# Performance work log

Hardware: AMD Instinct MI355X
Metric: run time of the kernel (lower is better)

## Reference

```python
import jax, jax.numpy as jnp
import numpy as np

N = 4096        # num_node == num_hyperedge
IN_FT = 512
OUT_FT = 512
COS_THR = 0.5
COS_K = 10
SCALER = 1.0
EPS = 1e-12  # torch F.normalize eps


def _kaiming_uniform(key, shape, fan_in, a=2.0):
    # kaiming_uniform_ with a=sqrt(4)=2: gain = sqrt(2/(1+a^2)), bound = gain*sqrt(3/fan_in)
    gain = np.sqrt(2.0 / (1.0 + a * a))
    bound = gain * np.sqrt(3.0 / fan_in)
    return jax.random.uniform(key, shape, jnp.float32, -bound, bound)


def setup_inputs() -> dict:
    key = jax.random.key(0)
    k_x, k_w1, k_w2, k_pw, k_pb = jax.random.split(key, 5)
    x = jax.random.normal(k_x, (N, IN_FT), jnp.float32)
    H = jnp.ones((N, N), jnp.float32)  # initial full incidence, sparsified in forward
    weight1 = jnp.abs(_kaiming_uniform(k_w1, (N, N), fan_in=N))
    weight2 = jnp.abs(_kaiming_uniform(k_w2, (N, N), fan_in=N))
    proj_w = _kaiming_uniform(k_pw, (OUT_FT, IN_FT), fan_in=IN_FT)
    b = 1.0 / np.sqrt(IN_FT)
    proj_b = jax.random.uniform(k_pb, (OUT_FT,), jnp.float32, -b, b)
    return {"x": x, "H": H, "proj_w": proj_w, "proj_b": proj_b,
            "weight1": weight1, "weight2": weight2}


def reference(x, H, proj_w, proj_b, weight1, weight2):
    # --- dynamic hypergraph construction: cosine similarity + threshold/top-k mask ---
    xn = x / jnp.maximum(jnp.linalg.norm(x, axis=1, keepdims=True), 1e-12)
    cos = xn @ xn.T                                  # [N, N]
    mask = cos > COS_THR
    _, idx = jax.lax.top_k(cos, COS_K)               # [N, K] top-k per row
    rows = jnp.arange(N)[:, None]
    mask = mask.at[rows, idx].set(True)
    Hm = H * mask.astype(H.dtype)                    # sparsified incidence

    # --- projection ---
    h = x @ proj_w.T + proj_b                        # [N, out_ft]

    # --- node -> hyperedge aggregation ---
    nw = (weight1 * Hm).T                            # [E, N]
    nw = nw / jnp.maximum(jnp.sum(jnp.abs(nw), axis=1, keepdims=True), EPS) * SCALER
    h = nw @ h                                       # [E, out_ft]

    # --- hyperedge -> node aggregation ---
    hw = weight2 * Hm                                # [N, E]
    hw = hw / jnp.maximum(jnp.sum(jnp.abs(hw), axis=1, keepdims=True), EPS) * SCALER
    return hw @ h                                    # [N, out_ft]
```

## Files before the change

kernel.cpp:

```cpp
#include <hip/hip_runtime.h>
#include <hip/hip_bf16.h>
#include <math.h>

#define N 4096
#define IN_FT 512
#define OUT_FT 512
#define COS_THR 0.5f
#define COS_K 10
#define EPSN 1e-12f
#define CAP 256
#define NW (N / 32)
#define CAP_C 128
#define GAPWIN 2e-4f
#define CNB 32
#define T0 0.08f
#define CAPT 512

typedef short s16x8 __attribute__((ext_vector_type(8)));
typedef float f32x4 __attribute__((ext_vector_type(4)));

__device__ __forceinline__ unsigned short f2bf(float f) {
    unsigned u = __float_as_uint(f);
    u += 0x7fff + ((u >> 16) & 1);
    return (unsigned short)(u >> 16);
}
__device__ __forceinline__ float bf2f(unsigned short h) {
    return __uint_as_float(((unsigned)h) << 16);
}
__device__ __forceinline__ void gload_lds16(const void* g, void* l) {
    __builtin_amdgcn_global_load_lds(
        (const __attribute__((address_space(1))) void*)g,
        (__attribute__((address_space(3))) void*)l, 16, 0, 0);
}

__global__ __launch_bounds__(256) void rownorm_k(const float* __restrict__ x,
                                                 unsigned short* __restrict__ xnh,
                                                 unsigned short* __restrict__ xnl,
                                                 float* __restrict__ norminv,
                                                 float* __restrict__ nrm) {
    int row = blockIdx.x;
    const float* xr = x + (size_t)row * IN_FT;
    float s = 0.f;
    for (int j = threadIdx.x; j < IN_FT; j += 256) { float v = xr[j]; s += v * v; }
    __shared__ float red[256];
    red[threadIdx.x] = s; __syncthreads();
    for (int off = 128; off > 0; off >>= 1) {
        if (threadIdx.x < off) red[threadIdx.x] += red[threadIdx.x + off];
        __syncthreads();
    }
    float nr = fmaxf(sqrtf(red[0]), 1e-12f);
    float inv = 1.0f / nr;
    if (threadIdx.x == 0) { norminv[row] = inv; nrm[row] = nr; }
    for (int j = threadIdx.x; j < IN_FT; j += 256) {
        float v = xr[j] * inv;
        unsigned short hi = f2bf(v);
        unsigned short lo = f2bf(v - bf2f(hi));
        xnh[(size_t)row * IN_FT + j] = hi;
        xnl[(size_t)row * IN_FT + j] = lo;
    }
}

__global__ __launch_bounds__(256) void cos_gemm_k(const unsigned short* __restrict__ xh,
                                                  const unsigned short* __restrict__ xl,
                                                  float* __restrict__ C) {
    __shared__ __align__(16) unsigned short As[2][128 * 32];
    __shared__ __align__(16) unsigned short Bs[2][128 * 32];
    int bid = blockIdx.x;
    int t = (bid & 7) * 66 + (bid >> 3);
    int by = 0;
    while (t >= CNB - by) { t -= CNB - by; ++by; }
    int bx = by + t;
    int tid = threadIdx.x;
    int wave = tid >> 6, l = tid & 63;
    int bi = by * 128, bj = bx * 128;
    int wm = wave >> 1, wn = wave & 1;
    int lm0 = wm * 64, ln0 = wn * 64;
    int lr4 = l >> 2;
    int lc4s = (((l & 3) ^ ((l >> 3) & 3)) * 8);
    int lr = l & 15, lg = l >> 4;
    int kqs = (((l >> 4) ^ ((l >> 1) & 3)) * 8);
    f32x4 acc[4][4] = {};
    int buf = 0;
#pragma unroll
    for (int q = 0; q < 2; ++q) {
        int r0 = (wave + q * 4) * 16;
        gload_lds16(xh + (size_t)(bi + r0 + lr4) * IN_FT + lc4s, &As[0][r0 * 32]);
        gload_lds16(xh + (size_t)(bj + r0 + lr4) * IN_FT + lc4s, &Bs[0][r0 * 32]);
    }
    asm volatile("s_waitcnt vmcnt(0)" ::: "memory");
    __syncthreads();
    for (int kt = 0; kt < 48; ++kt) {
        if (kt + 1 < 48) {
            int p = (kt + 1) >> 4;
            int kc = ((kt + 1) & 15) * 32;
            const unsigned short* sa = (p == 2) ? xl : xh;
            const unsigned short* sb = (p == 1) ? xl : xh;
#pragma unroll
            for (int q = 0; q < 2; ++q) {
                int r0 = (wave + q * 4) * 16;
                gload_lds16(sa + (size_t)(bi + r0 + lr4) * IN_FT + kc + lc4s,
                            &As[buf ^ 1][r0 * 32]);
                gload_lds16(sb + (size_t)(bj + r0 + lr4) * IN_FT + kc + lc4s,
                            &Bs[buf ^ 1][r0 * 32]);
            }
        }
        s16x8 a[4], b[4];
#pragma unroll
        for (int mi = 0; mi < 4; ++mi)
            a[mi] = *(const s16x8*)&As[buf][(lm0 + mi * 16 + lr) * 32 + kqs];
#pragma unroll
        for (int ni = 0; ni < 4; ++ni)
            b[ni] = *(const s16x8*)&Bs[buf][(ln0 + ni * 16 + lr) * 32 + kqs];
#pragma unroll
        for (int mi = 0; mi < 4; ++mi)
#pragma unroll
            for (int ni = 0; ni < 4; ++ni)
                acc[mi][ni] = __builtin_amdgcn_mfma_f32_16x16x32_bf16(a[mi], b[ni], acc[mi][ni], 0, 0, 0);
        asm volatile("s_waitcnt vmcnt(0)" ::: "memory");
        __syncthreads();
        buf ^= 1;
    }
#pragma unroll
    for (int mi = 0; mi < 4; ++mi)
#pragma unroll
        for (int r = 0; r < 4; ++r) {
            int m = bi + lm0 + mi * 16 + lg * 4 + r;
#pragma unroll
            for (int ni = 0; ni < 4; ++ni)
                C[(size_t)m * N + bj + ln0 + ni * 16 + lr] = acc[mi][ni][r];
        }
    if (bx != by) {
#pragma unroll
        for (int ni = 0; ni < 4; ++ni) {
            int cc = bj + ln0 + ni * 16 + lr;
#pragma unroll
            for (int mi = 0; mi < 4; ++mi) {
                float4 s = make_float4(acc[mi][ni][0], acc[mi][ni][1],
                                       acc[mi][ni][2], acc[mi][ni][3]);
                *(float4*)&C[(size_t)cc * N + bi + lm0 + mi * 16 + lg * 4] = s;
            }
        }
    }
}

__global__ __launch_bounds__(256) void topk_fix_k(const float* __restrict__ cosm,
                                                  const float* __restrict__ x,
                                                  const float* __restrict__ norminv,
                                                  unsigned* __restrict__ maskT,
                                                  const float* __restrict__ w2,
                                                  const float* __restrict__ Hmat,
                                                  int* __restrict__ rlist,
                                                  float* __restrict__ rval,
                                                  int* __restrict__ rcnt) {
    int row = blockIdx.x;
    int tid = threadIdx.x;
    int lane = tid & 63, wid = tid >> 6;
    __shared__ float wv[4][10];
    __shared__ int   wi[4][10];
    __shared__ int   win[10];
    __shared__ float v10s;
    __shared__ int   wtot[4];
    __shared__ int   wtotc[4];
    __shared__ int   wamb[4];
    __shared__ int   cj[CAP_C];
    __shared__ float exv[CAP_C];
    __shared__ unsigned char sel2[CAP_C];
    __shared__ float cv2[CAPT];
    __shared__ int   ci2[CAPT];
    const float* crow = cosm + (size_t)row * N;
    float v[16];
    unsigned fl = 0;
#pragma unroll
    for (int q = 0; q < 4; ++q) {
        float4 f4 = *(const float4*)&crow[tid * 16 + q * 4];
        v[q * 4 + 0] = f4.x; v[q * 4 + 1] = f4.y;
        v[q * 4 + 2] = f4.z; v[q * 4 + 3] = f4.w;
    }
#pragma unroll
    for (int c = 0; c < 16; ++c)
        if (v[c] > COS_THR) fl |= 1u << c;
    unsigned pm = 0;
#pragma unroll
    for (int c = 0; c < 16; ++c)
        if (v[c] > T0) pm |= 1u << c;
    {
        int pcnt = __popc(pm);
        int pscan = pcnt;
#pragma unroll
        for (int off = 1; off < 64; off <<= 1) {
            int nv = __shfl_up(pscan, off);
            if (lane >= off) pscan += nv;
        }
        if (lane == 63) wtotc[wid] = pscan;
        __syncthreads();
        int pbase = pscan - pcnt;
        for (int w = 0; w < wid; ++w) pbase += wtotc[w];
        unsigned m = pm; int pos = pbase;
        while (m) {
            int c = __builtin_ctz(m); m &= m - 1;
            if (pos < CAPT) { cv2[pos] = v[c]; ci2[pos] = tid * 16 + c; }
            ++pos;
        }
    }
    __syncthreads();
    int Mc = wtotc[0] + wtotc[1] + wtotc[2] + wtotc[3];
    bool fast = (Mc >= COS_K && Mc <= CAPT);
    if (fast) {
        if (wid == 0) {
            float cv[8]; int ci[8];
            int Kc = (Mc + 63) >> 6;
#pragma unroll
            for (int s = 0; s < 8; ++s) {
                int p = s * 64 + lane;
                bool ok = (s < Kc) && (p < Mc);
                cv[s] = ok ? cv2[p] : -INFINITY;
                ci[s] = ok ? ci2[p] : 0x7fffffff;
            }
            unsigned exm = 0;
            for (int t = 0; t < COS_K; ++t) {
                float best = -INFINITY; int bidx = 0x7fffffff;
#pragma unroll
                for (int s = 0; s < 8; ++s)
                    if (!((exm >> s) & 1) && cv[s] > best) { best = cv[s]; bidx = ci[s]; }
#pragma unroll
                for (int off = 32; off > 0; off >>= 1) {
                    float v2 = __shfl_xor(best, off);
                    int   i2 = __shfl_xor(bidx, off);
                    if (v2 > best || (v2 == best && i2 < bidx)) { best = v2; bidx = i2; }
                }
#pragma unroll
                for (int s = 0; s < 8; ++s)
                    if (ci[s] == bidx) exm |= 1u << s;
                if (lane == 0) { win[t] = bidx; if (t == COS_K - 1) v10s = best; }
            }
        }
        __syncthreads();
    } else {
        unsigned exm = 0;
#pragma unroll
        for (int t = 0; t < COS_K; ++t) {
            float best = -INFINITY; int bidx = 0x7fffffff;
#pragma unroll
            for (int c = 0; c < 16; ++c)
                if (!((exm >> c) & 1) && v[c] > best) { best = v[c]; bidx = tid * 16 + c; }
#pragma unroll
            for (int off = 32; off > 0; off >>= 1) {
                float v2 = __shfl_xor(best, off);
                int   i2 = __shfl_xor(bidx, off);
                if (v2 > best || (v2 == best && i2 < bidx)) { best = v2; bidx = i2; }
            }
            if ((bidx >> 4) == tid) exm |= 1u << (bidx & 15);
            if (lane == t) { wv[wid][t] = best; wi[wid][t] = bidx; }
        }
        __syncthreads();
        if (wid == 0) {
            float mv = -INFINITY; int mi = 0x7fffffff;
            if (lane < 40) { int g = lane / 10, s = lane - g * 10; mv = wv[g][s]; mi = wi[g][s]; }
            for (int t = 0; t < COS_K; ++t) {
                float best = mv; int bidx = mi;
#pragma unroll
                for (int off = 32; off > 0; off >>= 1) {
                    float v2 = __shfl_xor(best, off);
                    int   i2 = __shfl_xor(bidx, off);
                    if (v2 > best || (v2 == best && i2 < bidx)) { best = v2; bidx = i2; }
                }
                if (mi == bidx) mv = -INFINITY;
                if (lane == 0) { win[t] = bidx; if (t == COS_K - 1) v10s = best; }
            }
        }
        __syncthreads();
    }
    unsigned sel = 0;
#pragma unroll
    for (int t = 0; t < COS_K; ++t) {
        int wj = win[t];
        if ((wj >> 4) == tid) sel |= 1u << (wj & 15);
    }
    fl |= sel;
    float v10 = v10s;
    bool amb = false;
#pragma unroll
    for (int c = 0; c < 16; ++c) {
        if ((sel >> c) & 1) continue;
        float vc = v[c];
        if (vc > v10 - GAPWIN || fabsf(vc - COS_THR) < GAPWIN) amb = true;
    }
    unsigned long long ab = __ballot(amb);
    if (lane == 0) wamb[wid] = (ab != 0ull) ? 1 : 0;
    __syncthreads();
    bool blockamb = (wamb[0] | wamb[1] | wamb[2] | wamb[3]) != 0;
    if (blockamb) {
        unsigned cm = 0;
#pragma unroll
        for (int c = 0; c < 16; ++c)
            if (v[c] > v10 - GAPWIN || fabsf(v[c] - COS_THR) < GAPWIN) cm |= 1u << c;
        int ccnt = __popc(cm);
        int cscan = ccnt;
#pragma unroll
        for (int off = 1; off < 64; off <<= 1) {
            int nv = __shfl_up(cscan, off);
            if (lane >= off) cscan += nv;
        }
        if (lane == 63) wtot[wid] = cscan;
        __syncthreads();
        int cbase = cscan - ccnt;
        for (int w = 0; w < wid; ++w) cbase += wtot[w];
        {
            unsigned m = cm; int pos = cbase;
            while (m) {
                int c = __builtin_ctz(m); m &= m - 1;
                if (pos < CAP_C) cj[pos] = tid * 16 + c;
                ++pos;
            }
        }
        __syncthreads();
        int Mtot = wtot[0] + wtot[1] + wtot[2] + wtot[3];
        int M = Mtot < CAP_C ? Mtot : CAP_C;
        if (tid < M) {
            int j = cj[tid];
            float invr = norminv[row], invj = norminv[j];
            const float* xr = x + (size_t)row * IN_FT;
            const float* xj = x + (size_t)j * IN_FT;
            float acc = 0.f;
            for (int k = 0; k < IN_FT; ++k)
                acc = fmaf(xr[k] * invr, xj[k] * invj, acc);
            exv[tid] = acc;
        }
        __syncthreads();
        if (tid < M) {
            float vv = exv[tid]; int j = cj[tid];
            int rank = 0;
            for (int m2 = 0; m2 < M; ++m2) {
                float v2 = exv[m2]; int j2 = cj[m2];
                if (v2 > vv || (v2 == vv && j2 < j)) ++rank;
            }
            sel2[tid] = (rank < COS_K) ? 1 : 0;
        }
        __syncthreads();
        unsigned newfl = 0;
        {
            unsigned m = cm; int pos = cbase;
            unsigned done = 0;
            while (m) {
                int c = __builtin_ctz(m); m &= m - 1;
                bool f;
                if (pos < CAP_C) f = (exv[pos] > COS_THR) || sel2[pos];
                else             f = (v[c] > COS_THR);
                if (f) newfl |= 1u << c;
                done |= 1u << c;
                ++pos;
            }
#pragma unroll
            for (int c = 0; c < 16; ++c)
                if (!((done >> c) & 1) && v[c] > COS_THR) newfl |= 1u << c;
        }
        fl = newfl;
        __syncthreads();
    }
    unsigned flp = __shfl_xor(fl, 1);
    if (!(tid & 1))
        maskT[(size_t)(tid >> 1) * N + row] = (fl & 0xffffu) | (flp << 16);
    int cnt = __popc(fl);
    int scan = cnt;
#pragma unroll
    for (int off = 1; off < 64; off <<= 1) {
        int nv = __shfl_up(scan, off);
        if (lane >= off) scan += nv;
    }
    if (lane == 63) wtot[wid] = scan;
    __syncthreads();
    int base = scan - cnt;
    for (int w = 0; w < wid; ++w) base += wtot[w];
    unsigned m = fl;
    int pos = base;
    while (m) {
        int c = __builtin_ctz(m); m &= m - 1;
        int j = tid * 16 + c;
        if (pos < CAP) {
            size_t ofs = (size_t)row * N + j;
            rlist[(size_t)row * CAP + pos] = j;
            rval[(size_t)row * CAP + pos] = w2[ofs] * Hmat[ofs];
        }
        ++pos;
    }
    if (tid == 0) {
        int tot = wtot[0] + wtot[1] + wtot[2] + wtot[3];
        rcnt[row] = tot < CAP ? tot : CAP;
    }
}

__global__ __launch_bounds__(256) void cast_w_k(const float* __restrict__ w,
                                                unsigned short* __restrict__ wh,
                                                unsigned short* __restrict__ wl) {
    int i4 = blockIdx.x * 256 + threadIdx.x;
    float4 f = ((const float4*)w)[i4];
    ushort4 hi, lo;
    hi.x = f2bf(f.x); lo.x = f2bf(f.x - bf2f(hi.x));
    hi.y = f2bf(f.y); lo.y = f2bf(f.y - bf2f(hi.y));
    hi.z = f2bf(f.z); lo.z = f2bf(f.z - bf2f(hi.z));
    hi.w = f2bf(f.w); lo.w = f2bf(f.w - bf2f(hi.w));
    ((ushort4*)wh)[i4] = hi;
    ((ushort4*)wl)[i4] = lo;
}

__global__ __launch_bounds__(256) void proj_mfma_k(const unsigned short* __restrict__ xh,
                                                   const unsigned short* __restrict__ xl,
                                                   const unsigned short* __restrict__ wh,
                                                   const unsigned short* __restrict__ wl,
                                                   const float* __restrict__ bias,
                                                   const float* __restrict__ nrm,
                                                   float* __restrict__ h) {
    int tid = threadIdx.x;
    int wave = tid >> 6, l = tid & 63;
    int m0 = blockIdx.y * 64 + wave * 16;
    int n0 = blockIdx.x * 64;
    int lr = l & 15;
    int kq = (l >> 4) * 8;
    const unsigned short* pah = xh + (size_t)(m0 + lr) * IN_FT + kq;
    const unsigned short* pal = xl + (size_t)(m0 + lr) * IN_FT + kq;
    f32x4 acc[4] = {};
    for (int k0 = 0; k0 < IN_FT; k0 += 32) {
        s16x8 ah = *(const s16x8*)(pah + k0);
        s16x8 al = *(const s16x8*)(pal + k0);
#pragma unroll
        for (int g = 0; g < 4; ++g) {
            const unsigned short* pbh = wh + (size_t)(n0 + g * 16 + lr) * IN_FT + kq + k0;
            const unsigned short* pbl = wl + (size_t)(n0 + g * 16 + lr) * IN_FT + kq + k0;
            s16x8 bh = *(const s16x8*)pbh;
            s16x8 bl = *(const s16x8*)pbl;
            acc[g] = __builtin_amdgcn_mfma_f32_16x16x32_bf16(ah, bh, acc[g], 0, 0, 0);
            acc[g] = __builtin_amdgcn_mfma_f32_16x16x32_bf16(ah, bl, acc[g], 0, 0, 0);
            acc[g] = __builtin_amdgcn_mfma_f32_16x16x32_bf16(al, bh, acc[g], 0, 0, 0);
        }
    }
#pragma unroll
    for (int g = 0; g < 4; ++g)
#pragma unroll
        for (int r = 0; r < 4; ++r) {
            int m = m0 + (l >> 4) * 4 + r;
            int n = n0 + g * 16 + lr;
            h[(size_t)m * OUT_FT + n] = nrm[m] * acc[g][r] + bias[n];
        }
}

__global__ __launch_bounds__(256) void count_cols_k(const unsigned* __restrict__ maskT,
                                                    int* __restrict__ cnt16) {
    __shared__ unsigned ch[8][256];
    int tid = threadIdx.x;
    int eb = blockIdx.x, chunk = blockIdx.y;
    int wbase = eb * 8, v0 = chunk * 256;
#pragma unroll
    for (int i = 0; i < 8; ++i)
        ch[i][tid] = maskT[(size_t)(wbase + i) * N + v0 + tid];
    __syncthreads();
    int wl = tid >> 5, bp = tid & 31;
    int cnt = 0;
#pragma unroll 8
    for (int v = 0; v < 256; ++v) cnt += (ch[wl][v] >> bp) & 1;
    cnt16[chunk * N + eb * 256 + tid] = cnt;
}

__global__ __launch_bounds__(256) void fill_cols_k(const unsigned* __restrict__ maskT,
                                                   const int* __restrict__ cnt16,
                                                   const float* __restrict__ w1,
                                                   const float* __restrict__ Hmat,
                                                   int* __restrict__ elist,
                                                   float* __restrict__ eval_,
                                                   int* __restrict__ ecnt) {
    __shared__ unsigned ch[8][256];
    int tid = threadIdx.x;
    int eb = blockIdx.x, chunk = blockIdx.y;
    int e = eb * 256 + tid;
    int wbase = eb * 8, v0 = chunk * 256;
#pragma unroll
    for (int i = 0; i < 8; ++i)
        ch[i][tid] = maskT[(size_t)(wbase + i) * N + v0 + tid];
    int pos = 0;
    for (int c = 0; c < chunk; ++c) pos += cnt16[c * N + e];
    __syncthreads();
    int wl = tid >> 5;
    unsigned bit = 1u << (tid & 31);
    for (int v = 0; v < 256; ++v) {
        if (ch[wl][v] & bit) {
            if (pos < CAP) {
                size_t ofs = (size_t)(v0 + v) * N + e;
                elist[(size_t)e * CAP + pos] = v0 + v;
                eval_[(size_t)e * CAP + pos] = w1[ofs] * Hmat[ofs];
            }
            ++pos;
        }
    }
    if (chunk == 15) ecnt[e] = pos < CAP ? pos : CAP;
}

__global__ __launch_bounds__(256) void spmm_k(const int* __restrict__ list,
                                              const float* __restrict__ val,
                                              const int* __restrict__ cnt,
                                              const float* __restrict__ src,
                                              float* __restrict__ dst) {
    int i = blockIdx.x;
    int f2 = threadIdx.x;
    int c = cnt[i];
    float ssum = 0.f;
    for (int t = 0; t < c; ++t) ssum += fabsf(val[(size_t)i * CAP + t]);
    float acc0 = 0.f, acc1 = 0.f;
    for (int t = 0; t < c; ++t) {
        int j = list[(size_t)i * CAP + t];
        float a = val[(size_t)i * CAP + t];
        float2 s = *(const float2*)&src[(size_t)j * OUT_FT + f2 * 2];
        acc0 += a * s.x;
        acc1 += a * s.y;
    }
    float sc = 1.0f / fmaxf(ssum, EPSN);
    float2 o = make_float2(acc0 * sc, acc1 * sc);
    *(float2*)&dst[(size_t)i * OUT_FT + f2 * 2] = o;
}

extern "C" void kernel_launch(void* const* d_in, const int* in_sizes, int n_in,
                              void* d_out, int out_size, void* d_ws, size_t ws_size,
                              hipStream_t stream) {
    const float* x      = (const float*)d_in[0];
    const float* Hmat   = (const float*)d_in[1];
    const float* proj_w = (const float*)d_in[2];
    const float* proj_b = (const float*)d_in[3];
    const float* w1     = (const float*)d_in[4];
    const float* w2     = (const float*)d_in[5];
    float* out = (float*)d_out;

    char* ws = (char*)d_ws;
    unsigned short* xnh   = (unsigned short*)(ws + 0);
    unsigned short* xnl   = (unsigned short*)(ws + 4194304);
    float*          cosm  = (float*)(ws + 8388608);
    int*            elist = (int*)  (ws + 8388608);
    float*          eval_ = (float*)(ws + 12582912);
    float*          h     = (float*)(ws + 25165824);
    float*          h2    = (float*)(ws + 33554432);
    unsigned short* whi   = (unsigned short*)(ws + 50331648);
    unsigned short* wlo   = (unsigned short*)(ws + 50855936);
    unsigned*       maskT = (unsigned*)(ws + 75497472);
    int*            ecnt    = (int*)(ws + 77594624);
    int*            rcnt    = (int*)(ws + 77611008);
    float*          norminv = (float*)(ws + 77627392);
    float*          nrm     = (float*)(ws + 77643776);
    int*            rlist   = (int*)(ws + 77676544);
    float*          rval    = (float*)(ws + 81870848);
    int*            cnt16   = (int*)(ws + 86065152);

    rownorm_k<<<N, 256, 0, stream>>>(x, xnh, xnl, norminv, nrm);
    cos_gemm_k<<<CNB * (CNB + 1) / 2, 256, 0, stream>>>(xnh, xnl, cosm);
    topk_fix_k<<<N, 256, 0, stream>>>(cosm, x, norminv, maskT, w2, Hmat,
                                      rlist, rval, rcnt);
    cast_w_k<<<256, 256, 0, stream>>>(proj_w, whi, wlo);
    proj_mfma_k<<<dim3(OUT_FT / 64, N / 64), 256, 0, stream>>>(xnh, xnl, whi, wlo,
                                                               proj_b, nrm, h);
    count_cols_k<<<dim3(16, 16), 256, 0, stream>>>(maskT, cnt16);
    fill_cols_k<<<dim3(16, 16), 256, 0, stream>>>(maskT, cnt16, w1, Hmat, elist, eval_, ecnt);
    spmm_k<<<N, 256, 0, stream>>>(elist, eval_, ecnt, h, h2);
    spmm_k<<<N, 256, 0, stream>>>(rlist, rval, rcnt, h2, out);
}
```

Baseline: 269.4 us.

## Emit top-k candidates from cosine GEMM epilogue and split top-k into fast/fallback

The cosine GEMM epilogue now appends every value above a low threshold to a per-row candidate list using atomics. A new fast top-k kernel works only on these compact lists instead of rereading the full 4096-wide cosine row, and flags rows that need the old full-row path. A separate fallback kernel runs the original logic only for flagged rows. This trades a full read of the cosine matrix for scattered atomics in the GEMM epilogue plus an extra kernel launch, and lowers the candidate capacity, which may send more rows to the fallback.

```diff
diff --git a/kernel.cpp b/kernel.cpp
--- a/kernel.cpp
+++ b/kernel.cpp
@@ -14,7 +14,7 @@
 #define GAPWIN 2e-4f
 #define CNB 32
 #define T0 0.08f
-#define CAPT 512
+#define CAPT 192
 
 typedef short s16x8 __attribute__((ext_vector_type(8)));
 typedef float f32x4 __attribute__((ext_vector_type(4)));
@@ -37,7 +37,9 @@
                                                  unsigned short* __restrict__ xnh,
                                                  unsigned short* __restrict__ xnl,
                                                  float* __restrict__ norminv,
-                                                 float* __restrict__ nrm) {
+                                                 float* __restrict__ nrm,
+                                                 int* __restrict__ ccnt,
+                                                 int* __restrict__ fbflag) {
     int row = blockIdx.x;
     const float* xr = x + (size_t)row * IN_FT;
     float s = 0.f;
@@ -50,7 +52,7 @@
     }
     float nr = fmaxf(sqrtf(red[0]), 1e-12f);
     float inv = 1.0f / nr;
-    if (threadIdx.x == 0) { norminv[row] = inv; nrm[row] = nr; }
+    if (threadIdx.x == 0) { norminv[row] = inv; nrm[row] = nr; ccnt[row] = 0; fbflag[row] = 0; }
     for (int j = threadIdx.x; j < IN_FT; j += 256) {
         float v = xr[j] * inv;
         unsigned short hi = f2bf(v);
@@ -62,7 +64,10 @@
 
 __global__ __launch_bounds__(256) void cos_gemm_k(const unsigned short* __restrict__ xh,
                                                   const unsigned short* __restrict__ xl,
-                                                  float* __restrict__ C) {
+                                                  float* __restrict__ C,
+                                                  int* __restrict__ ccnt,
+                                                  float* __restrict__ cval,
+                                                  int* __restrict__ cidx) {
     __shared__ __align__(16) unsigned short As[2][128 * 32];
     __shared__ __align__(16) unsigned short Bs[2][128 * 32];
     int bid = blockIdx.x;
@@ -126,8 +131,18 @@
         for (int r = 0; r < 4; ++r) {
             int m = bi + lm0 + mi * 16 + lg * 4 + r;
 #pragma unroll
-            for (int ni = 0; ni < 4; ++ni)
-                C[(size_t)m * N + bj + ln0 + ni * 16 + lr] = acc[mi][ni][r];
+            for (int ni = 0; ni < 4; ++ni) {
+                float val = acc[mi][ni][r];
+                int n = bj + ln0 + ni * 16 + lr;
+                C[(size_t)m * N + n] = val;
+                if (val > T0) {
+                    int p = atomicAdd(&ccnt[m], 1);
+                    if (p < CAPT) {
+                        cval[(size_t)m * CAPT + p] = val;
+                        cidx[(size_t)m * CAPT + p] = n;
+                    }
+                }
+            }
         }
     if (bx != by) {
 #pragma unroll
@@ -138,21 +153,182 @@
                 float4 s = make_float4(acc[mi][ni][0], acc[mi][ni][1],
                                        acc[mi][ni][2], acc[mi][ni][3]);
                 *(float4*)&C[(size_t)cc * N + bi + lm0 + mi * 16 + lg * 4] = s;
-            }
-        }
-    }
-}
-
-__global__ __launch_bounds__(256) void topk_fix_k(const float* __restrict__ cosm,
-                                                  const float* __restrict__ x,
-                                                  const float* __restrict__ norminv,
-                                                  unsigned* __restrict__ maskT,
-                                                  const float* __restrict__ w2,
-                                                  const float* __restrict__ Hmat,
-                                                  int* __restrict__ rlist,
-                                                  float* __restrict__ rval,
-                                                  int* __restrict__ rcnt) {
+#pragma unroll
+                for (int r = 0; r < 4; ++r) {
+                    float val = acc[mi][ni][r];
+                    if (val > T0) {
+                        int p = atomicAdd(&ccnt[cc], 1);
+                        if (p < CAPT) {
+                            cval[(size_t)cc * CAPT + p] = val;
+                            cidx[(size_t)cc * CAPT + p] = bi + lm0 + mi * 16 + lg * 4 + r;
+                        }
+                    }
+                }
+            }
+        }
+    }
+}
+
+__global__ __launch_bounds__(256) void topk_fast_k(const float* __restrict__ cval,
+                                                   const int* __restrict__ cidx,
+                                                   const int* __restrict__ ccnt,
+                                                   const float* __restrict__ x,
+                                                   const float* __restrict__ norminv,
+                                                   unsigned* __restrict__ maskT,
+                                                   const float* __restrict__ w2,
+                                                   const float* __restrict__ Hmat,
+                                                   int* __restrict__ rlist,
+                                                   float* __restrict__ rval,
+                                                   int* __restrict__ rcnt,
+                                                   int* __restrict__ fbflag) {
+    int row = blockIdx.x, tid = threadIdx.x;
+    int lane = tid & 63, wid = tid >> 6;
+    __shared__ int   win[10];
+    __shared__ float v10s;
+    __shared__ int   wred[4];
+    __shared__ int   cjp[CAP_C];
+    __shared__ int   cjj[CAP_C];
+    __shared__ float exv[CAP_C];
+    __shared__ unsigned char selw[CAP_C];
+    __shared__ unsigned char candflag[CAPT];
+    __shared__ unsigned ldsmask[NW];
+    int Mc = ccnt[row];
+    if (Mc < COS_K || Mc > CAPT) { if (tid == 0) fbflag[row] = 1; return; }
+    if (wid == 0) {
+        float cv[3]; int ci[3];
+#pragma unroll
+        for (int s = 0; s < 3; ++s) {
+            int p = s * 64 + lane;
+            bool ok = p < Mc;
+            cv[s] = ok ? cval[(size_t)row * CAPT + p] : -INFINITY;
+            ci[s] = ok ? cidx[(size_t)row * CAPT + p] : 0x7fffffff;
+        }
+        unsigned exm = 0;
+        for (int t = 0; t < COS_K; ++t) {
+            float best = -INFINITY; int bidx = 0x7fffffff;
+#pragma unroll
+            for (int s = 0; s < 3; ++s)
+                if (!((exm >> s) & 1) &&
+                    (cv[s] > best || (cv[s] == best && ci[s] < bidx))) { best = cv[s]; bidx = ci[s]; }
+#pragma unroll
+            for (int off = 32; off > 0; off >>= 1) {
+                float v2 = __shfl_xor(best, off);
+                int   i2 = __shfl_xor(bidx, off);
+                if (v2 > best || (v2 == best && i2 < bidx)) { best = v2; bidx = i2; }
+            }
+#pragma unroll
+            for (int s = 0; s < 3; ++s)
+                if (ci[s] == bidx) exm |= 1u << s;
+            if (lane == 0) { win[t] = bidx; if (t == COS_K - 1) v10s = best; }
+        }
+    }
+    __syncthreads();
+    float v10 = v10s;
+    if (v10 - GAPWIN <= T0) { if (tid == 0) fbflag[row] = 1; return; }
+    bool valid = tid < Mc;
+    float myv = 0.f; int myj = -1;
+    if (valid) {
+        myv = cval[(size_t)row * CAPT + tid];
+        myj = cidx[(size_t)row * CAPT + tid];
+    }
+    bool isw = valid && ((myv > v10 - GAPWIN) || (fabsf(myv - COS_THR) < GAPWIN));
+    unsigned long long wb = __ballot(isw);
+    if (lane == 0) wred[wid] = __popcll(wb);
+    __syncthreads();
+    int Mw = wred[0] + wred[1] + wred[2] + wred[3];
+    if (Mw > CAP_C) { if (tid == 0) fbflag[row] = 1; return; }
+    bool inwin = false;
+    if (valid) {
+#pragma unroll
+        for (int t = 0; t < COS_K; ++t) if (win[t] == myj) inwin = true;
+        candflag[tid] = ((myv > COS_THR) || inwin) ? 1 : 0;
+    }
+    bool amb = Mw > COS_K;
+    if (amb) {
+        int pb = isw ? 1 : 0;
+        int scan = pb;
+#pragma unroll
+        for (int off = 1; off < 64; off <<= 1) {
+            int nv = __shfl_up(scan, off);
+            if (lane >= off) scan += nv;
+        }
+        int base = scan - pb;
+        for (int w = 0; w < wid; ++w) base += wred[w];
+        if (pb) cjp[base] = tid;
+        __syncthreads();
+        if (tid < Mw) {
+            int j = cidx[(size_t)row * CAPT + cjp[tid]];
+            cjj[tid] = j;
+            float invr = norminv[row], invj = norminv[j];
+            const float* xr = x + (size_t)row * IN_FT;
+            const float* xj = x + (size_t)j * IN_FT;
+            float acc = 0.f;
+            for (int k = 0; k < IN_FT; ++k)
+                acc = fmaf(xr[k] * invr, xj[k] * invj, acc);
+            exv[tid] = acc;
+        }
+        __syncthreads();
+        if (tid < Mw) {
+            float vv = exv[tid]; int j = cjj[tid];
+            int rank = 0;
+            for (int m2 = 0; m2 < Mw; ++m2) {
+                float v2 = exv[m2]; int j2 = cjj[m2];
+                if (v2 > vv || (v2 == vv && j2 < j)) ++rank;
+            }
+            selw[tid] = (rank < COS_K) ? 1 : 0;
+        }
+        __syncthreads();
+        if (tid < Mw)
+            candflag[cjp[tid]] = ((exv[tid] > COS_THR) || selw[tid]) ? 1 : 0;
+    }
+    __syncthreads();
+    if (tid < NW) ldsmask[tid] = 0;
+    __syncthreads();
+    if (valid && candflag[tid]) atomicOr(&ldsmask[myj >> 5], 1u << (myj & 31));
+    __syncthreads();
+    if (tid < NW) maskT[(size_t)tid * N + row] = ldsmask[tid];
+    unsigned word = 0; int cnt = 0;
+    if (tid < NW) { word = ldsmask[tid]; cnt = __popc(word); }
+    int scan2 = cnt;
+#pragma unroll
+    for (int off = 1; off < 64; off <<= 1) {
+        int nv = __shfl_up(scan2, off);
+        if (lane >= off) scan2 += nv;
+    }
+    if (lane == 63) wred[wid] = scan2;
+    __syncthreads();
+    if (tid < NW) {
+        int base2 = scan2 - cnt + (wid == 1 ? wred[0] : 0);
+        unsigned m = word; int pos = base2;
+        while (m) {
+            int b = __builtin_ctz(m); m &= m - 1;
+            int j = tid * 32 + b;
+            if (pos < CAP) {
+                size_t ofs = (size_t)row * N + j;
+                rlist[(size_t)row * CAP + pos] = j;
+                rval[(size_t)row * CAP + pos] = w2[ofs] * Hmat[ofs];
+            }
+            ++pos;
+        }
+    }
+    if (tid == 0) {
+        int tot = wred[0] + wred[1];
+        rcnt[row] = tot < CAP ? tot : CAP;
+    }
+}
+
+__global__ __launch_bounds__(256) void topk_fb_k(const int* __restrict__ fbflag,
+                                                 const float* __restrict__ cosm,
+                                                 const float* __restrict__ x,
+                                                 const float* __restrict__ norminv,
+                                                 unsigned* __restrict__ maskT,
+                                                 const float* __restrict__ w2,
+                                                 const float* __restrict__ Hmat,
+                                                 int* __restrict__ rlist,
+                                                 float* __restrict__ rval,
+                                                 int* __restrict__ rcnt) {
     int row = blockIdx.x;
+    if (!fbflag[row]) return;
     int tid = threadIdx.x;
     int lane = tid & 63, wid = tid >> 6;
     __shared__ float wv[4][10];
@@ -160,13 +336,10 @@
     __shared__ int   win[10];
     __shared__ float v10s;
     __shared__ int   wtot[4];
-    __shared__ int   wtotc[4];
     __shared__ int   wamb[4];
     __shared__ int   cj[CAP_C];
     __shared__ float exv[CAP_C];
     __shared__ unsigned char sel2[CAP_C];
-    __shared__ float cv2[CAPT];
-    __shared__ int   ci2[CAPT];
     const float* crow = cosm + (size_t)row * N;
     float v[16];
     unsigned fl = 0;
@@ -179,97 +352,39 @@
 #pragma unroll
     for (int c = 0; c < 16; ++c)
         if (v[c] > COS_THR) fl |= 1u << c;
-    unsigned pm = 0;
-#pragma unroll
-    for (int c = 0; c < 16; ++c)
-        if (v[c] > T0) pm |= 1u << c;
-    {
-        int pcnt = __popc(pm);
-        int pscan = pcnt;
-#pragma unroll
-        for (int off = 1; off < 64; off <<= 1) {
-            int nv = __shfl_up(pscan, off);
-            if (lane >= off) pscan += nv;
-        }
-        if (lane == 63) wtotc[wid] = pscan;
-        __syncthreads();
-        int pbase = pscan - pcnt;
-        for (int w = 0; w < wid; ++w) pbase += wtotc[w];
-        unsigned m = pm; int pos = pbase;
-        while (m) {
-            int c = __builtin_ctz(m); m &= m - 1;
-            if (pos < CAPT) { cv2[pos] = v[c]; ci2[pos] = tid * 16 + c; }
-            ++pos;
-        }
-    }
-    __syncthreads();
-    int Mc = wtotc[0] + wtotc[1] + wtotc[2] + wtotc[3];
-    bool fast = (Mc >= COS_K && Mc <= CAPT);
-    if (fast) {
-        if (wid == 0) {
-            float cv[8]; int ci[8];
-            int Kc = (Mc + 63) >> 6;
-#pragma unroll
-            for (int s = 0; s < 8; ++s) {
-                int p = s * 64 + lane;
-                bool ok = (s < Kc) && (p < Mc);
-                cv[s] = ok ? cv2[p] : -INFINITY;
-                ci[s] = ok ? ci2[p] : 0x7fffffff;
-            }
-            unsigned exm = 0;
-            for (int t = 0; t < COS_K; ++t) {
-                float best = -INFINITY; int bidx = 0x7fffffff;
-#pragma unroll
-                for (int s = 0; s < 8; ++s)
-                    if (!((exm >> s) & 1) && cv[s] > best) { best = cv[s]; bidx = ci[s]; }
-#pragma unroll
-                for (int off = 32; off > 0; off >>= 1) {
-                    float v2 = __shfl_xor(best, off);
-                    int   i2 = __shfl_xor(bidx, off);
-                    if (v2 > best || (v2 == best && i2 < bidx)) { best = v2; bidx = i2; }
-                }
-#pragma unroll
-                for (int s = 0; s < 8; ++s)
-                    if (ci[s] == bidx) exm |= 1u << s;
-                if (lane == 0) { win[t] = bidx; if (t == COS_K - 1) v10s = best; }
-            }
-        }
-        __syncthreads();
-    } else {
-        unsigned exm = 0;
-#pragma unroll
+    unsigned exm = 0;
+#pragma unroll
+    for (int t = 0; t < COS_K; ++t) {
+        float best = -INFINITY; int bidx = 0x7fffffff;
+#pragma unroll
+        for (int c = 0; c < 16; ++c)
+            if (!((exm >> c) & 1) && v[c] > best) { best = v[c]; bidx = tid * 16 + c; }
+#pragma unroll
+        for (int off = 32; off > 0; off >>= 1) {
+            float v2 = __shfl_xor(best, off);
+            int   i2 = __shfl_xor(bidx, off);
+            if (v2 > best || (v2 == best && i2 < bidx)) { best = v2; bidx = i2; }
+        }
+        if ((bidx >> 4) == tid) exm |= 1u << (bidx & 15);
+        if (lane == t) { wv[wid][t] = best; wi[wid][t] = bidx; }
+    }
+    __syncthreads();
+    if (wid == 0) {
+        float mv = -INFINITY; int mi = 0x7fffffff;
+        if (lane < 40) { int g = lane / 10, s = lane - g * 10; mv = wv[g][s]; mi = wi[g][s]; }
         for (int t = 0; t < COS_K; ++t) {
-            float best = -INFINITY; int bidx = 0x7fffffff;
-#pragma unroll
-            for (int c = 0; c < 16; ++c)
-                if (!((exm >> c) & 1) && v[c] > best) { best = v[c]; bidx = tid * 16 + c; }
+            float best = mv; int bidx = mi;
 #pragma unroll
             for (int off = 32; off > 0; off >>= 1) {
                 float v2 = __shfl_xor(best, off);
                 int   i2 = __shfl_xor(bidx, off);
                 if (v2 > best || (v2 == best && i2 < bidx)) { best = v2; bidx = i2; }
             }
-            if ((bidx >> 4) == tid) exm |= 1u << (bidx & 15);
-            if (lane == t) { wv[wid][t] = best; wi[wid][t] = bidx; }
-        }
-        __syncthreads();
-        if (wid == 0) {
-            float mv = -INFINITY; int mi = 0x7fffffff;
-            if (lane < 40) { int g = lane / 10, s = lane - g * 10; mv = wv[g][s]; mi = wi[g][s]; }
-            for (int t = 0; t < COS_K; ++t) {
-                float best = mv; int bidx = mi;
-#pragma unroll
-                for (int off = 32; off > 0; off >>= 1) {
-                    float v2 = __shfl_xor(best, off);
-                    int   i2 = __shfl_xor(bidx, off);
-                    if (v2 > best || (v2 == best && i2 < bidx)) { best = v2; bidx = i2; }
-                }
-                if (mi == bidx) mv = -INFINITY;
-                if (lane == 0) { win[t] = bidx; if (t == COS_K - 1) v10s = best; }
-            }
-        }
-        __syncthreads();
-    }
+            if (mi == bidx) mv = -INFINITY;
+            if (lane == 0) { win[t] = bidx; if (t == COS_K - 1) v10s = best; }
+        }
+    }
+    __syncthreads();
     unsigned sel = 0;
 #pragma unroll
     for (int t = 0; t < COS_K; ++t) {
@@ -294,8 +409,8 @@
 #pragma unroll
         for (int c = 0; c < 16; ++c)
             if (v[c] > v10 - GAPWIN || fabsf(v[c] - COS_THR) < GAPWIN) cm |= 1u << c;
-        int ccnt = __popc(cm);
-        int cscan = ccnt;
+        int ccnt2 = __popc(cm);
+        int cscan = ccnt2;
 #pragma unroll
         for (int off = 1; off < 64; off <<= 1) {
             int nv = __shfl_up(cscan, off);
@@ -303,7 +418,7 @@
         }
         if (lane == 63) wtot[wid] = cscan;
         __syncthreads();
-        int cbase = cscan - ccnt;
+        int cbase = cscan - ccnt2;
         for (int w = 0; w < wid; ++w) cbase += wtot[w];
         {
             unsigned m = cm; int pos = cbase;
@@ -537,19 +652,25 @@
     float*          h2    = (float*)(ws + 33554432);
     unsigned short* whi   = (unsigned short*)(ws + 50331648);
     unsigned short* wlo   = (unsigned short*)(ws + 50855936);
+    int*            cnt16 = (int*)(ws + 52428800);
     unsigned*       maskT = (unsigned*)(ws + 75497472);
     int*            ecnt    = (int*)(ws + 77594624);
     int*            rcnt    = (int*)(ws + 77611008);
     float*          norminv = (float*)(ws + 77627392);
     float*          nrm     = (float*)(ws + 77643776);
-    int*            rlist   = (int*)(ws + 77676544);
-    float*          rval    = (float*)(ws + 81870848);
-    int*            cnt16   = (int*)(ws + 86065152);
-
-    rownorm_k<<<N, 256, 0, stream>>>(x, xnh, xnl, norminv, nrm);
-    cos_gemm_k<<<CNB * (CNB + 1) / 2, 256, 0, stream>>>(xnh, xnl, cosm);
-    topk_fix_k<<<N, 256, 0, stream>>>(cosm, x, norminv, maskT, w2, Hmat,
-                                      rlist, rval, rcnt);
+    int*            fbflag  = (int*)(ws + 77660160);
+    int*            ccnt    = (int*)(ws + 77676544);
+    int*            rlist   = (int*)(ws + 77692928);
+    float*          rval    = (float*)(ws + 81887232);
+    float*          cval    = (float*)(ws + 86081536);
+    int*            cidx    = (int*)(ws + 89227264);
+
+    rownorm_k<<<N, 256, 0, stream>>>(x, xnh, xnl, norminv, nrm, ccnt, fbflag);
+    cos_gemm_k<<<CNB * (CNB + 1) / 2, 256, 0, stream>>>(xnh, xnl, cosm, ccnt, cval, cidx);
+    topk_fast_k<<<N, 256, 0, stream>>>(cval, cidx, ccnt, x, norminv, maskT,
+                                       w2, Hmat, rlist, rval, rcnt, fbflag);
+    topk_fb_k<<<N, 256, 0, stream>>>(fbflag, cosm, x, norminv, maskT,
+                                     w2, Hmat, rlist, rval, rcnt);
     cast_w_k<<<256, 256, 0, stream>>>(proj_w, whi, wlo);
     proj_mfma_k<<<dim3(OUT_FT / 64, N / 64), 256, 0, stream>>>(xnh, xnl, whi, wlo,
                                                                proj_b, nrm, h);
```

Result: slower. 409.2 us (+51.9%).
